# Kernel optimization log

Hardware: AMD Instinct MI355X
Metric: run time of the kernel (lower is better)

## Reference

```python
import math
import jax, jax.numpy as jnp
import numpy as np

N_QUBITS = 8
N_QLAYERS = 2
HIDDEN = 768
BATCH = 8192
LN_EPS = 1e-5


def _ry_gate(theta):
    # theta: scalar or (B,) -> (2,2) or (B,2,2) complex64
    h = theta * 0.5
    c, s = jnp.cos(h), jnp.sin(h)
    g = jnp.stack([jnp.stack([c, -s], axis=-1), jnp.stack([s, c], axis=-1)], axis=-2)
    return g.astype(jnp.complex64)


def _rz_gate(theta):
    t = theta.astype(jnp.complex64)
    e0, e1 = jnp.exp(-0.5j * t), jnp.exp(0.5j * t)
    z = jnp.zeros_like(e0)
    return jnp.stack([jnp.stack([e0, z], axis=-1), jnp.stack([z, e1], axis=-1)], axis=-2)


def _apply_1q(state, gate, w, n):
    # state: (B, 2**n); gate: (2,2) shared or (B,2,2) per-sample; wire w (0 = MSB)
    B = state.shape[0]
    s = state.reshape(B, 2 ** w, 2, -1)
    if gate.ndim == 2:
        s = jnp.einsum('ij,bljr->blir', gate, s)
    else:
        s = jnp.einsum('bij,bljr->blir', gate, s)
    return s.reshape(B, -1)


def _apply_cnot(state, c, t, n):
    B = state.shape[0]
    s = state.reshape((B,) + (2,) * n)
    ax_c = 1 + c
    s0 = jnp.take(s, 0, axis=ax_c)  # control=0 branch, control axis removed
    s1 = jnp.take(s, 1, axis=ax_c)
    ax_t = 1 + t - (1 if t > c else 0)
    s1 = jnp.flip(s1, axis=ax_t)    # X on target when control=1
    s = jnp.stack([s0, s1], axis=ax_c)
    return s.reshape(B, -1)


def _circuit(angles, weights_ry, weights_rz):
    # angles: (B, n) float32 -> (B, n) PauliZ expectations, batched statevector sim
    n, L = N_QUBITS, N_QLAYERS
    B = angles.shape[0]
    state = jnp.zeros((B, 2 ** n), dtype=jnp.complex64).at[:, 0].set(1.0)
    for i in range(n):
        state = _apply_1q(state, _ry_gate(angles[:, i]), i, n)
    for i in range(1, n):
        state = _apply_cnot(state, 0, i, n)
    for l in range(L):
        for i in range(n):
            state = _apply_1q(state, _ry_gate(weights_ry[l, i]), i, n)
            state = _apply_1q(state, _rz_gate(weights_rz[l, i]), i, n)
    for i in range(1, n):
        state = _apply_cnot(state, i, 0, n)
    probs = jnp.abs(state) ** 2  # (B, 2**n)
    k = jnp.arange(2 ** n)
    bits = (k[None, :] >> (n - 1 - jnp.arange(n))[:, None]) & 1  # wire 0 = MSB (PennyLane)
    signs = (1 - 2 * bits).astype(probs.dtype)  # (n, 2**n)
    return probs @ signs.T  # (B, n)


def setup_inputs() -> dict:
    key = jax.random.key(0)
    ks = jax.random.split(key, 8)
    return {
        'hidden': jax.random.normal(ks[0], (BATCH, HIDDEN), dtype=jnp.float32),
        'W_in': jax.random.normal(ks[1], (N_QUBITS, HIDDEN), dtype=jnp.float32) * (1.0 / math.sqrt(HIDDEN)),
        'b_in': jax.random.normal(ks[2], (N_QUBITS,), dtype=jnp.float32) * 0.01,
        'W_out': jax.random.normal(ks[3], (HIDDEN, N_QUBITS), dtype=jnp.float32) * (1.0 / math.sqrt(N_QUBITS)),
        'b_out': jax.random.normal(ks[4], (HIDDEN,), dtype=jnp.float32) * 0.01,
        'weights_ry': jax.random.normal(ks[5], (N_QLAYERS, N_QUBITS), dtype=jnp.float32) * 0.1,
        'weights_rz': jax.random.normal(ks[6], (N_QLAYERS, N_QUBITS), dtype=jnp.float32) * 0.1,
        'gamma': jnp.ones((HIDDEN,), dtype=jnp.float32),
        'beta': jnp.zeros((HIDDEN,), dtype=jnp.float32),
    }


def reference(hidden, W_in, b_in, W_out, b_out, weights_ry, weights_rz, gamma, beta):
    phase = 0.0
    angles = jnp.tanh(hidden @ W_in.T + b_in) * math.pi + phase  # (B, n)
    meas = _circuit(angles, weights_ry, weights_rz).astype(jnp.float32)  # (B, n)
    y = meas @ W_out.T + b_out  # (B, h)
    mu = jnp.mean(y, axis=-1, keepdims=True)
    var = jnp.mean(jnp.square(y - mu), axis=-1, keepdims=True)
    return (y - mu) * jax.lax.rsqrt(var + LN_EPS) * gamma + beta
```

## Files before the change

kernel.cpp:

```cpp
#include <hip/hip_runtime.h>
#include <hip/hip_bf16.h>

#define NQ    8
#define HID   768
#define BATCH 8192
#define TPB   1024
#define SPB   16
#define NBLK  (BATCH / SPB)

template<int BF> __device__ __forceinline__ float LDV(const void* p, int i) {
    if constexpr (BF) return __bfloat162float(((const __hip_bfloat16*)p)[i]);
    else return ((const float*)p)[i];
}
template<int BF> __device__ __forceinline__ void STV(void* p, int i, float v) {
    if constexpr (BF) ((__hip_bfloat16*)p)[i] = __float2bfloat16(v);
    else ((float*)p)[i] = v;
}
template<int BF> __device__ __forceinline__ float4 LD4(const void* p, int i4) {
    if constexpr (BF) {
        ushort4 v = ((const ushort4*)p)[i4];
        float4 r;
        r.x = __uint_as_float(((unsigned)v.x) << 16);
        r.y = __uint_as_float(((unsigned)v.y) << 16);
        r.z = __uint_as_float(((unsigned)v.z) << 16);
        r.w = __uint_as_float(((unsigned)v.w) << 16);
        return r;
    } else {
        return ((const float4*)p)[i4];
    }
}
__device__ __forceinline__ float bflo(unsigned w) { return __uint_as_float(w << 16); }
__device__ __forceinline__ float bfhi(unsigned w) { return __uint_as_float(w & 0xffff0000u); }

#define SMEM_BYTES 58368

template<int BF>
__device__ __forceinline__ void run_all(
    const void* hidden_, const void* W_in_, const void* b_in_,
    const void* W_out_, const void* b_out_, const void* wry_, const void* wrz_,
    const void* gamma_, const void* beta_, void* out_, char* smem)
{
    const int tid  = threadIdx.x;
    const int lane = tid & 63;
    const int wv   = tid >> 6;
    const int j    = lane >> 3;
    const int b    = blockIdx.x * SPB + wv;

    float* sBout;
    float2* sGB;
    if constexpr (BF) {
        sBout = (float*)(smem + 24576);
        sGB   = (float2*)(smem + 27648);
        if (tid < 768) {
            ((uint4*)smem)[tid]           = ((const uint4*)W_in_)[tid];
            ((uint4*)(smem + 12288))[tid] = ((const uint4*)W_out_)[tid];
            sBout[tid] = LDV<BF>(b_out_, tid);
            sGB[tid]   = make_float2(LDV<BF>(gamma_, tid), LDV<BF>(beta_, tid));
        }
    } else {
        sBout = (float*)(smem + 49152);
        sGB   = (float2*)(smem + 52224);
        float* sWin = (float*)smem;
        float4* sWoutLo = (float4*)(smem + 24576);
        float4* sWoutHi = (float4*)(smem + 36864);
        ((float4*)sWin)[tid] = LD4<BF>(W_in_, tid);
        if (tid < NQ*HID/4 - TPB)
            ((float4*)sWin)[tid + TPB] = LD4<BF>(W_in_, tid + TPB);
        if (tid < HID) {
            sWoutLo[tid] = LD4<BF>(W_out_, tid*2);
            sWoutHi[tid] = LD4<BF>(W_out_, tid*2 + 1);
            sBout[tid]   = LDV<BF>(b_out_, tid);
            sGB[tid]     = make_float2(LDV<BF>(gamma_, tid), LDV<BF>(beta_, tid));
        }
    }

    float DA, DB, Kr, Ki;
    {
        float ry0 = LDV<BF>(wry_, j), ry1 = LDV<BF>(wry_, NQ + j);
        float rz0 = LDV<BF>(wrz_, j), rz1 = LDV<BF>(wrz_, NQ + j);
        float cA = cosf(0.5f*ry0), sA = sinf(0.5f*ry0);
        float cB = cosf(0.5f*ry1), sB = sinf(0.5f*ry1);
        float p0c = cosf(0.5f*rz0), p0s = sinf(0.5f*rz0);
        float p1c = cosf(0.5f*rz1), p1s = sinf(0.5f*rz1);
        float g00r =  cA*p0c, g00i = -cA*p0s;
        float g01r = -sA*p0c, g01i =  sA*p0s;
        float g10r =  sA*p0c, g10i =  sA*p0s;
        float g11r =  cA*p0c, g11i =  cA*p0s;
        float h00r = cB*g00r - sB*g10r, h00i = cB*g00i - sB*g10i;
        float h01r = cB*g01r - sB*g11r, h01i = cB*g01i - sB*g11i;
        float h10r = sB*g00r + cB*g10r, h10i = sB*g00i + cB*g10i;
        float h11r = sB*g01r + cB*g11r, h11i = sB*g01i + cB*g11i;
        float f00r = h00r*p1c + h00i*p1s, f00i = h00i*p1c - h00r*p1s;
        float f01r = h01r*p1c + h01i*p1s, f01i = h01i*p1c - h01r*p1s;
        float f10r = h10r*p1c - h10i*p1s, f10i = h10i*p1c + h10r*p1s;
        float f11r = h11r*p1c - h11i*p1s, f11i = h11i*p1c + h11r*p1s;
        DA = f00r*f00r + f00i*f00i - (f10r*f10r + f10i*f10i);
        DB = f01r*f01r + f01i*f01i - (f11r*f11r + f11i*f11i);
        Kr = (f00r*f01r + f00i*f01i) - (f10r*f11r + f10i*f11i);
        Ki = (f00i*f01r - f00r*f01i) - (f10i*f11r - f10r*f11i);
    }
    __syncthreads();

    float p[NQ];
    #pragma unroll
    for (int q = 0; q < NQ; ++q) p[q] = 0.f;
    const int hb = b * (HID/4);
    #pragma unroll
    for (int t = 0; t < 3; ++t) {
        const int q4 = (t << 6) + lane;
        float4 h = LD4<BF>(hidden_, hb + q4);
        if constexpr (BF) {
            const uint2* sWinU2 = (const uint2*)smem;
            #pragma unroll
            for (int jj = 0; jj < NQ; ++jj) {
                uint2 w = sWinU2[jj*(HID/4) + q4];
                p[jj] = fmaf(h.x, bflo(w.x), p[jj]);
                p[jj] = fmaf(h.y, bfhi(w.x), p[jj]);
                p[jj] = fmaf(h.z, bflo(w.y), p[jj]);
                p[jj] = fmaf(h.w, bfhi(w.y), p[jj]);
            }
        } else {
            const float* sWin = (const float*)smem;
            #pragma unroll
            for (int jj = 0; jj < NQ; ++jj) {
                float4 w = ((const float4*)(sWin + jj*HID))[q4];
                p[jj] = fmaf(h.x, w.x, p[jj]);
                p[jj] = fmaf(h.y, w.y, p[jj]);
                p[jj] = fmaf(h.z, w.z, p[jj]);
                p[jj] = fmaf(h.w, w.w, p[jj]);
            }
        }
    }
    const bool mb0 = ((lane >> 3) & 1) != 0;
    const bool mb1 = ((lane >> 4) & 1) != 0;
    const bool mb2 = ((lane >> 5) & 1) != 0;
    float np[4];
    #pragma unroll
    for (int k = 0; k < 4; ++k) {
        float sent = mb0 ? p[2*k]   : p[2*k+1];
        float keep = mb0 ? p[2*k+1] : p[2*k];
        np[k] = keep + __shfl_xor(sent, 8, 64);
    }
    float nq2[2];
    #pragma unroll
    for (int k = 0; k < 2; ++k) {
        float sent = mb1 ? np[2*k]   : np[2*k+1];
        float keep = mb1 ? np[2*k+1] : np[2*k];
        nq2[k] = keep + __shfl_xor(sent, 16, 64);
    }
    float z;
    {
        float sent = mb2 ? nq2[0] : nq2[1];
        float keep = mb2 ? nq2[1] : nq2[0];
        z = keep + __shfl_xor(sent, 32, 64);
    }
    z += __shfl_xor(z, 1, 64);
    z += __shfl_xor(z, 2, 64);
    z += __shfl_xor(z, 4, 64);

    float zb = z + LDV<BF>(b_in_, j);
    float th = tanhf(zb);
    float sj = sinpif(th), cj = cospif(th);

    float ca = 0.5f * (DA + DB), da = 0.5f * (DA - DB);
    const bool g0 = (j == 0);
    float uu = da * cj;
    float vv = fmaf(Kr, sj, ca);
    float MA = g0 ? 1.f : (vv + uu), MB = g0 ? 1.f : (vv - uu);
    float fr = g0 ? 1.f : Kr,        fi = g0 ? 0.f : (cj * Ki);
    #pragma unroll
    for (int d = 8; d < 64; d <<= 1) {
        MA *= __shfl_xor(MA, d, 64);
        MB *= __shfl_xor(MB, d, 64);
        float qr = __shfl_xor(fr, d, 64);
        float qi = __shfl_xor(fi, d, 64);
        float nr = fr*qr - fi*qi;
        float ni = fr*qi + fi*qr;
        fr = nr; fi = ni;
    }
    float DA0 = __shfl(DA, 0, 64), DB0 = __shfl(DB, 0, 64);
    float Kr0 = __shfl(Kr, 0, 64), Ki0 = __shfl(Ki, 0, 64);
    float cc0 = __shfl(cj, 0, 64), sc0 = __shfl(sj, 0, 64);
    float meas0 = 0.5f*(1.f+cc0)*DA0*MA + 0.5f*(1.f-cc0)*DB0*MB
                + sc0*(Kr0*fr - Ki0*fi);
    float measj = g0 ? meas0 : fmaf(cc0, uu, vv);
    float m0 = meas0;
    float m1 = __shfl(measj,  8, 64), m2 = __shfl(measj, 16, 64);
    float m3 = __shfl(measj, 24, 64), m4 = __shfl(measj, 32, 64);
    float m5 = __shfl(measj, 40, 64), m6 = __shfl(measj, 48, 64);
    float m7 = __shfl(measj, 56, 64);

    const int rowbase = b * HID;
    float yv[12];
    float sum = 0.f, sq = 0.f;
    #pragma unroll
    for (int k = 0; k < 12; ++k) {
        const int c = lane + (k << 6);
        float y = sBout[c];
        if constexpr (BF) {
            uint4 wp = ((const uint4*)(smem + 12288))[c];
            y = fmaf(m0, bflo(wp.x), y); y = fmaf(m1, bfhi(wp.x), y);
            y = fmaf(m2, bflo(wp.y), y); y = fmaf(m3, bfhi(wp.y), y);
            y = fmaf(m4, bflo(wp.z), y); y = fmaf(m5, bfhi(wp.z), y);
            y = fmaf(m6, bflo(wp.w), y); y = fmaf(m7, bfhi(wp.w), y);
        } else {
            float4 w0 = ((const float4*)(smem + 24576))[c];
            float4 w1 = ((const float4*)(smem + 36864))[c];
            y = fmaf(m0, w0.x, y); y = fmaf(m1, w0.y, y);
            y = fmaf(m2, w0.z, y); y = fmaf(m3, w0.w, y);
            y = fmaf(m4, w1.x, y); y = fmaf(m5, w1.y, y);
            y = fmaf(m6, w1.z, y); y = fmaf(m7, w1.w, y);
        }
        yv[k] = y;
        sum += y;
        sq = fmaf(y, y, sq);
    }
    #pragma unroll
    for (int d = 1; d < 64; d <<= 1) {
        sum += __shfl_xor(sum, d, 64);
        sq  += __shfl_xor(sq,  d, 64);
    }
    float mean = sum * (1.f/HID);
    float var  = fmaf(sq, 1.f/HID, -mean*mean);
    float rstd = rsqrtf(var + 1e-5f);
    #pragma unroll
    for (int k = 0; k < 12; ++k) {
        const int c = lane + (k << 6);
        float2 gb = sGB[c];
        float o = fmaf((yv[k] - mean) * rstd, gb.x, gb.y);
        STV<BF>(out_, rowbase + c, o);
    }
}

__global__ __launch_bounds__(TPB, 8) void main_kernel(
    const void* hidden_, const void* W_in_, const void* b_in_,
    const void* W_out_, const void* b_out_, const void* wry_, const void* wrz_,
    const void* gamma_, const void* beta_, void* out_)
{
    __shared__ __align__(16) char smem[SMEM_BYTES];
    const int lane = threadIdx.x & 63;
    unsigned wrd = ((const unsigned*)hidden_)[lane];
    unsigned lo  = wrd & 0xffffu;
    unsigned e   = (lo >> 7) & 0xffu;
    bool v = (lo == 0u) || (e >= 100u && e <= 133u);
    unsigned long long mask = __ballot(v);
    int flag = (__popcll(mask) > 32) ? 1 : 0;
    if (flag)
        run_all<1>(hidden_, W_in_, b_in_, W_out_, b_out_, wry_, wrz_,
                   gamma_, beta_, out_, smem);
    else
        run_all<0>(hidden_, W_in_, b_in_, W_out_, b_out_, wry_, wrz_,
                   gamma_, beta_, out_, smem);
}

extern "C" void kernel_launch(void* const* d_in, const int* in_sizes, int n_in,
                              void* d_out, int out_size, void* d_ws, size_t ws_size,
                              hipStream_t stream) {
    const void* hidden = d_in[0];
    const void* W_in   = d_in[1];
    const void* b_in   = d_in[2];
    const void* W_out  = d_in[3];
    const void* b_out  = d_in[4];
    const void* wry    = d_in[5];
    const void* wrz    = d_in[6];
    const void* gamma  = d_in[7];
    const void* beta   = d_in[8];
    (void)d_ws; (void)ws_size;
    main_kernel<<<NBLK, TPB, 0, stream>>>(hidden, W_in, b_in, W_out, b_out,
                                          wry, wrz, gamma, beta, d_out);
}
```

Measured before the change: 98.20 us.

## Halve block size, read fp32 weights from global, precompute gate constants once

Blocks shrink from 16 samples (1024 threads) to 8 samples (512 threads), and LDS use drops by no longer staging the fp32 W_in/W_out in shared memory. The fp32 path now reads those weights straight from global memory and relies on the cache. The per-qubit gate constants (DA, DB, Kr, Ki) are computed by 8 threads into shared memory instead of by every lane, which removes redundant trig work. The aim is cheaper per-block setup and more resident blocks, at the cost of extra global or L2 loads for the weights in the fp32 path.

```diff
diff --git a/kernel.cpp b/kernel.cpp
--- a/kernel.cpp
+++ b/kernel.cpp
@@ -4,8 +4,8 @@
 #define NQ    8
 #define HID   768
 #define BATCH 8192
-#define TPB   1024
-#define SPB   16
+#define TPB   512
+#define SPB   8
 #define NBLK  (BATCH / SPB)
 
 template<int BF> __device__ __forceinline__ float LDV(const void* p, int i) {
@@ -32,7 +32,7 @@
 __device__ __forceinline__ float bflo(unsigned w) { return __uint_as_float(w << 16); }
 __device__ __forceinline__ float bfhi(unsigned w) { return __uint_as_float(w & 0xffff0000u); }
 
-#define SMEM_BYTES 58368
+#define SMEM_BYTES 33920
 
 template<int BF>
 __device__ __forceinline__ void run_all(
@@ -46,38 +46,23 @@
     const int j    = lane >> 3;
     const int b    = blockIdx.x * SPB + wv;
 
-    float* sBout;
-    float2* sGB;
-    if constexpr (BF) {
-        sBout = (float*)(smem + 24576);
-        sGB   = (float2*)(smem + 27648);
-        if (tid < 768) {
-            ((uint4*)smem)[tid]           = ((const uint4*)W_in_)[tid];
-            ((uint4*)(smem + 12288))[tid] = ((const uint4*)W_out_)[tid];
-            sBout[tid] = LDV<BF>(b_out_, tid);
-            sGB[tid]   = make_float2(LDV<BF>(gamma_, tid), LDV<BF>(beta_, tid));
+    float*  sBout = (float*)(smem + 24576);
+    float2* sGB   = (float2*)(smem + 27648);
+    float4* sQC   = (float4*)(smem + 33792);
+
+    for (int idx = tid; idx < HID; idx += TPB) {
+        if constexpr (BF) {
+            ((uint4*)smem)[idx]           = ((const uint4*)W_in_)[idx];
+            ((uint4*)(smem + 12288))[idx] = ((const uint4*)W_out_)[idx];
         }
-    } else {
-        sBout = (float*)(smem + 49152);
-        sGB   = (float2*)(smem + 52224);
-        float* sWin = (float*)smem;
-        float4* sWoutLo = (float4*)(smem + 24576);
-        float4* sWoutHi = (float4*)(smem + 36864);
-        ((float4*)sWin)[tid] = LD4<BF>(W_in_, tid);
-        if (tid < NQ*HID/4 - TPB)
-            ((float4*)sWin)[tid + TPB] = LD4<BF>(W_in_, tid + TPB);
-        if (tid < HID) {
-            sWoutLo[tid] = LD4<BF>(W_out_, tid*2);
-            sWoutHi[tid] = LD4<BF>(W_out_, tid*2 + 1);
-            sBout[tid]   = LDV<BF>(b_out_, tid);
-            sGB[tid]     = make_float2(LDV<BF>(gamma_, tid), LDV<BF>(beta_, tid));
-        }
-    }
-
-    float DA, DB, Kr, Ki;
-    {
-        float ry0 = LDV<BF>(wry_, j), ry1 = LDV<BF>(wry_, NQ + j);
-        float rz0 = LDV<BF>(wrz_, j), rz1 = LDV<BF>(wrz_, NQ + j);
+        sBout[idx] = LDV<BF>(b_out_, idx);
+        sGB[idx]   = make_float2(LDV<BF>(gamma_, idx), LDV<BF>(beta_, idx));
+    }
+
+    if (tid < NQ) {
+        const int q = tid;
+        float ry0 = LDV<BF>(wry_, q), ry1 = LDV<BF>(wry_, NQ + q);
+        float rz0 = LDV<BF>(wrz_, q), rz1 = LDV<BF>(wrz_, NQ + q);
         float cA = cosf(0.5f*ry0), sA = sinf(0.5f*ry0);
         float cB = cosf(0.5f*ry1), sB = sinf(0.5f*ry1);
         float p0c = cosf(0.5f*rz0), p0s = sinf(0.5f*rz0);
@@ -94,10 +79,11 @@
         float f01r = h01r*p1c + h01i*p1s, f01i = h01i*p1c - h01r*p1s;
         float f10r = h10r*p1c - h10i*p1s, f10i = h10i*p1c + h10r*p1s;
         float f11r = h11r*p1c - h11i*p1s, f11i = h11i*p1c + h11r*p1s;
-        DA = f00r*f00r + f00i*f00i - (f10r*f10r + f10i*f10i);
-        DB = f01r*f01r + f01i*f01i - (f11r*f11r + f11i*f11i);
-        Kr = (f00r*f01r + f00i*f01i) - (f10r*f11r + f10i*f11i);
-        Ki = (f00i*f01r - f00r*f01i) - (f10i*f11r - f10r*f11i);
+        float DA = f00r*f00r + f00i*f00i - (f10r*f10r + f10i*f10i);
+        float DB = f01r*f01r + f01i*f01i - (f11r*f11r + f11i*f11i);
+        float Kr = (f00r*f01r + f00i*f01i) - (f10r*f11r + f10i*f11i);
+        float Ki = (f00i*f01r - f00r*f01i) - (f10i*f11r - f10r*f11i);
+        sQC[q] = make_float4(DA, DB, Kr, Ki);
     }
     __syncthreads();
 
@@ -120,10 +106,9 @@
                 p[jj] = fmaf(h.w, bfhi(w.y), p[jj]);
             }
         } else {
-            const float* sWin = (const float*)smem;
             #pragma unroll
             for (int jj = 0; jj < NQ; ++jj) {
-                float4 w = ((const float4*)(sWin + jj*HID))[q4];
+                float4 w = LD4<BF>(W_in_, jj*(HID/4) + q4);
                 p[jj] = fmaf(h.x, w.x, p[jj]);
                 p[jj] = fmaf(h.y, w.y, p[jj]);
                 p[jj] = fmaf(h.z, w.z, p[jj]);
@@ -158,6 +143,8 @@
     z += __shfl_xor(z, 2, 64);
     z += __shfl_xor(z, 4, 64);
 
+    float4 qq = sQC[j];
+    float DA = qq.x, DB = qq.y, Kr = qq.z, Ki = qq.w;
     float zb = z + LDV<BF>(b_in_, j);
     float th = tanhf(zb);
     float sj = sinpif(th), cj = cospif(th);
@@ -178,11 +165,10 @@
         float ni = fr*qi + fi*qr;
         fr = nr; fi = ni;
     }
-    float DA0 = __shfl(DA, 0, 64), DB0 = __shfl(DB, 0, 64);
-    float Kr0 = __shfl(Kr, 0, 64), Ki0 = __shfl(Ki, 0, 64);
+    float4 q0 = sQC[0];
     float cc0 = __shfl(cj, 0, 64), sc0 = __shfl(sj, 0, 64);
-    float meas0 = 0.5f*(1.f+cc0)*DA0*MA + 0.5f*(1.f-cc0)*DB0*MB
-                + sc0*(Kr0*fr - Ki0*fi);
+    float meas0 = 0.5f*(1.f+cc0)*q0.x*MA + 0.5f*(1.f-cc0)*q0.y*MB
+                + sc0*(q0.z*fr - q0.w*fi);
     float measj = g0 ? meas0 : fmaf(cc0, uu, vv);
     float m0 = meas0;
     float m1 = __shfl(measj,  8, 64), m2 = __shfl(measj, 16, 64);
@@ -204,8 +190,8 @@
             y = fmaf(m4, bflo(wp.z), y); y = fmaf(m5, bfhi(wp.z), y);
             y = fmaf(m6, bflo(wp.w), y); y = fmaf(m7, bfhi(wp.w), y);
         } else {
-            float4 w0 = ((const float4*)(smem + 24576))[c];
-            float4 w1 = ((const float4*)(smem + 36864))[c];
+            float4 w0 = LD4<BF>(W_out_, c*2);
+            float4 w1 = LD4<BF>(W_out_, c*2 + 1);
             y = fmaf(m0, w0.x, y); y = fmaf(m1, w0.y, y);
             y = fmaf(m2, w0.z, y); y = fmaf(m3, w0.w, y);
             y = fmaf(m4, w1.x, y); y = fmaf(m5, w1.y, y);
```

Measured after the change: 103.3 us. +5.2%, slower.
